# Kernel tuning notes

Hardware: AMD Instinct MI355X
Metric: run time of the kernel (lower is better)

## Reference

```python
import jax, jax.numpy as jnp
import numpy as np

EPS = 1e-7
BLOCK = 64  # block_size from init_kwargs


def project(x):
    norm = jnp.clip(jnp.linalg.norm(x, axis=-1, keepdims=True), EPS)
    return jnp.where(norm >= 1.0, x / norm * (1.0 - EPS), x)


def mobius_add(x, y, c):
    x2 = jnp.sum(x * x, -1, keepdims=True)
    y2 = jnp.sum(y * y, -1, keepdims=True)
    xy = jnp.sum(x * y, -1, keepdims=True)
    num = (1 + 2 * c * xy + c * y2) * x + (1 - c * x2) * y
    den = 1 + 2 * c * xy + c * c * x2 * y2
    return project(num / jnp.clip(den, EPS))


def logmap0(y, c):
    sqrt_c = jnp.clip(jnp.sqrt(c), EPS)
    yn = jnp.linalg.norm(y, axis=-1, keepdims=True)
    mag = jnp.arctanh(jnp.minimum(yn, 1.0 - EPS)) / sqrt_c
    return jnp.where(yn < EPS, jnp.zeros_like(y), mag * (y / jnp.clip(yn, EPS)))


def expmap0(v, c):
    sqrt_c = jnp.clip(jnp.sqrt(c), EPS)
    vn = jnp.linalg.norm(v, axis=-1, keepdims=True)
    mag = jnp.tanh(sqrt_c * jnp.clip(vn, EPS)) / sqrt_c
    return project(jnp.where(vn < EPS, jnp.zeros_like(v), mag * (v / jnp.clip(vn, EPS))))


def pdist(x, y, c):
    # x: [B,H,S,1,D], y: [B,H,1,S,D], c: [1,H,1,1,1] -> [B,H,S,S]
    sqrt_c = jnp.clip(jnp.sqrt(c), EPS)
    add_norm = jnp.linalg.norm(mobius_add(-x, y, c), axis=-1)
    sc = jnp.squeeze(sqrt_c, -1)
    arg = jnp.minimum(sc * add_norm, 1.0 - EPS)
    return 2.0 * jnp.arctanh(arg) / sc


def layernorm(x, scale, bias, eps=1e-6):
    mu = jnp.mean(x, -1, keepdims=True)
    var = jnp.mean(jnp.square(x - mu), -1, keepdims=True)
    return (x - mu) * jax.lax.rsqrt(var + eps) * scale + bias


def precompute_freqs_cis(dim, end, theta=10000.0):
    f = 1.0 / theta ** (jnp.arange(0, dim, 2, dtype=jnp.float32) / dim)
    return jnp.exp(1j * jnp.outer(jnp.arange(end), f))


def rope(x, fc):
    # split-half rotary, as in WubuBlock.apply_rotary_emb
    xr, xi = jnp.split(x, 2, -1)
    xc = jax.lax.complex(xr, xi) * fc.reshape(1, 1, fc.shape[0], fc.shape[1])
    return jnp.concatenate([xc.real, xc.imag], -1)


def setup_inputs() -> dict:
    key = jax.random.key(0)
    ks = jax.random.split(key, 8)
    B, N, D, H = 1, 1024, 512, 8
    w = lambda k, shape, s=0.02: jax.random.normal(k, shape, jnp.float32) * s
    return {
        'x': w(ks[0], (B, N, D), 0.02),  # points well inside the Poincare ball
        'c_global': jax.random.uniform(ks[1], (B, 1), jnp.float32, 0.5, 1.5),
        'W_qkv': w(ks[2], (D, 3 * D)), 'b_qkv': jnp.zeros((3 * D,), jnp.float32),
        'W_out': w(ks[3], (D, D)), 'b_out': jnp.zeros((D,), jnp.float32),
        'ln1_scale': jnp.ones((D,), jnp.float32), 'ln1_bias': jnp.zeros((D,), jnp.float32),
        'ln2_scale': jnp.ones((D,), jnp.float32), 'ln2_bias': jnp.zeros((D,), jnp.float32),
        'W_ff1': w(ks[4], (D, 4 * D)), 'b_ff1': jnp.zeros((4 * D,), jnp.float32),
        'W_ff2': w(ks[5], (4 * D, D)), 'b_ff2': jnp.zeros((D,), jnp.float32),
        'c_per_head_logits': jnp.zeros((H,), jnp.float32),
        'geo_scale': jnp.ones((1, H, 1, 1), jnp.float32),
        'start_pos': 0,
    }


def reference(x, c_global, W_qkv, b_qkv, W_out, b_out, ln1_scale, ln1_bias,
              ln2_scale, ln2_bias, W_ff1, b_ff1, W_ff2, b_ff2,
              c_per_head_logits, geo_scale, start_pos):
    B, N, D = x.shape
    H = c_per_head_logits.shape[0]
    hd = D // H
    S = BLOCK
    nb = N // S
    Be = B * nb
    xb = x.reshape(Be, S, D)
    c_b = jnp.repeat(c_global, nb, axis=0).reshape(Be, 1, 1)

    # tangent-space layernorm (norm1) then logmap to tangent for QKV proj
    xn = expmap0(layernorm(logmap0(xb, c_b), ln1_scale, ln1_bias), c_b)
    xt = logmap0(xn, c_b)
    qkv = (xt @ W_qkv + b_qkv).reshape(Be, S, 3, H, hd).transpose(2, 0, 3, 1, 4)
    q, k, v = qkv[0], qkv[1], qkv[2]  # [Be,H,S,hd]

    fc = precompute_freqs_cis(hd, S)
    q = rope(q, fc)
    k = rope(k, fc)

    c_h = jax.nn.softplus(c_per_head_logits).reshape(1, H, 1, 1)
    qh = expmap0(q, c_h)
    kh = expmap0(k, c_h)

    # full pairwise hyperbolic distance: [Be,H,S,S]
    d = pdist(qh[:, :, :, None, :], kh[:, :, None, :, :], c_h[:, :, None, :, :])
    attn = jax.nn.softmax(-geo_scale * d, axis=-1)
    ao = jnp.einsum('bhqk,bhkd->bhqd', attn, v)
    ao = ao.transpose(0, 2, 1, 3).reshape(Be, S, D)

    ah = expmap0(ao @ W_out + b_out, c_b)
    xa = mobius_add(xb, ah, c_b)  # hyperbolic residual

    # hyperbolic FFN with tangent-space norm (norm2)
    xn2 = expmap0(layernorm(logmap0(xa, c_b), ln2_scale, ln2_bias), c_b)
    t = logmap0(xn2, c_b)
    fh = expmap0(jax.nn.gelu(t @ W_ff1 + b_ff1) @ W_ff2 + b_ff2, c_b)
    out = mobius_add(xa, fh, c_b)
    return out.reshape(B, N, D)
```

## Files before the change

kernel.cpp:

```cpp
#include <hip/hip_runtime.h>
#include <math.h>

#define DEV __device__ __forceinline__
typedef _Float16 h16;
typedef __attribute__((ext_vector_type(8))) _Float16 h8v;
typedef __attribute__((ext_vector_type(4))) _Float16 h4v;
typedef __attribute__((ext_vector_type(4))) float f4v;

constexpr int NTOK = 1024;
constexpr int D    = 512;
constexpr int H    = 8;
constexpr int NB   = 16;
constexpr double EPSd = 1e-7;

DEV double wave_sum(double v) {
#pragma unroll
  for (int m = 32; m; m >>= 1) v += __shfl_xor(v, m, 64);
  return v;
}

DEV void tcast64(const float* __restrict__ src, h16* __restrict__ dst,
                 int K, int N, int n0, int k0, float* tls ) {
  const int tx = threadIdx.x & 15, ty = threadIdx.x >> 4;
#pragma unroll
  for (int it = 0; it < 4; ++it) {
    const int k = ty + it * 16;
    float4 v = *(const float4*)(src + (size_t)(k0 + k) * N + n0 + tx * 4);
    *(float4*)(tls + k * 68 + tx * 4) = v;
  }
  __syncthreads();
#pragma unroll
  for (int it = 0; it < 4; ++it) {
    const int n = ty + it * 16;
    const int kc = tx * 4;
    h4v o;
#pragma unroll
    for (int j = 0; j < 4; ++j) o[j] = (h16)tls[(kc + j) * 68 + n];
    *(h4v*)(dst + (size_t)(n0 + n) * K + k0 + kc) = o;
  }
}

__global__ void k_prep(const float* __restrict__ Wqkv, const float* __restrict__ Wout,
                       const float* __restrict__ Wff1, const float* __restrict__ Wff2,
                       const float* __restrict__ x, const float* __restrict__ cg,
                       const float* __restrict__ s1, const float* __restrict__ b1,
                       h16* __restrict__ qT, h16* __restrict__ oT,
                       h16* __restrict__ f1T, h16* __restrict__ f2T,
                       h16* __restrict__ xt) {
  __shared__ __align__(16) float tls[64 * 68];
  const int bid = blockIdx.x;
  if (bid < 768) {
    const float* src; h16* dst; int K, N, bx, by, l;
    if (bid < 192)      { l = bid;       src = Wqkv; dst = qT;  K = 512;  N = 1536; bx = l % 24; by = l / 24; }
    else if (bid < 256) { l = bid - 192; src = Wout; dst = oT;  K = 512;  N = 512;  bx = l % 8;  by = l / 8;  }
    else if (bid < 512) { l = bid - 256; src = Wff1; dst = f1T; K = 512;  N = 2048; bx = l % 32; by = l / 32; }
    else                { l = bid - 512; src = Wff2; dst = f2T; K = 2048; N = 512;  bx = l % 8;  by = l / 8;  }
    tcast64(src, dst, K, N, bx * 64, by * 64, tls);
    return;
  }
  const int wid = threadIdx.x >> 6, lane = threadIdx.x & 63;
  const int tok = (bid - 768) * 4 + wid;
  const float4* xr = (const float4*)(x + (size_t)tok * D);
  float4 xv0 = xr[lane], xv1 = xr[lane + 64];
  double sv = 0.0, svv = 0.0;
  {
    const float e[8] = {xv0.x, xv0.y, xv0.z, xv0.w, xv1.x, xv1.y, xv1.z, xv1.w};
#pragma unroll
    for (int j = 0; j < 8; ++j) { double d = e[j]; sv += d; svv += d * d; }
  }
  sv = wave_sum(sv); svv = wave_sum(svv);
  double c = (double)cg[0];
  double sc = sqrt(c); if (sc < EPSd) sc = EPSd;
  double yn = sqrt(svv);
  double arg0 = yn; if (arg0 > 1.0 - EPSd) arg0 = 1.0 - EPSd;
  double f = (yn < EPSd) ? 0.0 : atanh(arg0) / sc / fmax(yn, EPSd);
  double mu = f * sv / D;
  double var = f * f * svv / D - mu * mu;
  double rs = 1.0 / sqrt(var + 1e-6);
  const float4* s1r = (const float4*)s1;
  const float4* b1r = (const float4*)b1;
  float4 sA = s1r[lane], sB = s1r[lane + 64];
  float4 bA = b1r[lane], bB = b1r[lane + 64];
  double w[8]; double sww = 0.0;
  {
    const float e[8]  = {xv0.x, xv0.y, xv0.z, xv0.w, xv1.x, xv1.y, xv1.z, xv1.w};
    const float se[8] = {sA.x, sA.y, sA.z, sA.w, sB.x, sB.y, sB.z, sB.w};
    const float be[8] = {bA.x, bA.y, bA.z, bA.w, bB.x, bB.y, bB.z, bB.w};
#pragma unroll
    for (int j = 0; j < 8; ++j) {
      w[j] = (f * (double)e[j] - mu) * rs * (double)se[j] + (double)be[j];
      sww += w[j] * w[j];
    }
  }
  sww = wave_sum(sww);
  double vn = sqrt(sww);
  double F = 0.0;
  if (vn >= EPSd) {
    double mag_e = tanh(sc * fmax(vn, EPSd)) / sc;
    F = atanh(fmin(mag_e, 1.0 - EPSd)) / (sc * vn);
  }
  h16* dst = xt + (size_t)tok * D;
#pragma unroll
  for (int half = 0; half < 2; ++half) {
    h4v o;
#pragma unroll
    for (int e = 0; e < 4; ++e) o[e] = (h16)(float)(F * w[half * 4 + e]);
    *(h4v*)(dst + 4 * (lane + 64 * half)) = o;
  }
}

DEV void stage_tile(const h16* __restrict__ gbase, int rowstride, h16* lds,
                    int wid, int lane) {
#pragma unroll
  for (int j = 0; j < 2; ++j) {
    const int rbase = wid * 16 + j * 8;
    const int grow = rbase + (lane >> 3);
    const int gch = (lane & 7) ^ (lane >> 3);
    const h16* gp = gbase + (size_t)grow * rowstride + gch * 8;
    __builtin_amdgcn_global_load_lds(
        (const __attribute__((address_space(1))) void*)gp,
        (__attribute__((address_space(3))) void*)(lds + rbase * 64), 16, 0, 0);
  }
}
DEV h8v read_frag(const h16* lds, int row, int c) {
  const int p = c ^ (row & 7);
  return *(const h8v*)(lds + row * 64 + p * 8);
}

template <int GELU, int OHALF, int SPLITK>
__global__ __launch_bounds__(256) void k_mm(
    const h16* __restrict__ A, const h16* __restrict__ B,
    const float* __restrict__ bias, float* __restrict__ Cf, h16* __restrict__ Ch,
    int M, int N, int K) {
  __shared__ __align__(16) h16 As[3][64 * 64];
  __shared__ __align__(16) h16 Bs[3][64 * 64];
  const int tid = threadIdx.x;
  const int lane = tid & 63, wid = tid >> 6;
  const int wr = (wid >> 1) * 32, wc = (wid & 1) * 32;
  const int lr = lane & 15, lg = lane >> 4;
  const size_t r0 = (size_t)blockIdx.y * 64, c0 = (size_t)blockIdx.x * 64;
  const int kz = SPLITK ? blockIdx.z : 0;
  const int Keff = SPLITK ? (K >> 1) : K;
  const f4v z = {0.f, 0.f, 0.f, 0.f};
  f4v acc[2][2]; acc[0][0] = z; acc[0][1] = z; acc[1][0] = z; acc[1][1] = z;
  const h16* Abase = A + r0 * K + (size_t)kz * Keff;
  const h16* Bbase = B + c0 * K + (size_t)kz * Keff;
  const int NT = Keff >> 6;
  stage_tile(Abase, K, As[0], wid, lane);
  stage_tile(Bbase, K, Bs[0], wid, lane);
  stage_tile(Abase + 64, K, As[1], wid, lane);
  stage_tile(Bbase + 64, K, Bs[1], wid, lane);
  int cur = 0;
  for (int t = 0; t < NT; ++t) {
    const int pre = (cur == 2) ? 0 : cur + 1;
    const int pre2 = (pre == 2) ? 0 : pre + 1;
    if (t + 2 < NT) {
      stage_tile(Abase + (t + 2) * 64, K, As[pre2], wid, lane);
      stage_tile(Bbase + (t + 2) * 64, K, Bs[pre2], wid, lane);
    }
    const int rem = NT - 1 - t;
    if (rem >= 2)      asm volatile("s_waitcnt vmcnt(8)" ::: "memory");
    else if (rem == 1) asm volatile("s_waitcnt vmcnt(4)" ::: "memory");
    else               asm volatile("s_waitcnt vmcnt(0)" ::: "memory");
    asm volatile("s_barrier" ::: "memory");
    const h16* Ac = As[cur];
    const h16* Bc = Bs[cur];
#pragma unroll
    for (int ks = 0; ks < 2; ++ks) {
      const int c = ks * 4 + lg;
      h8v a0 = read_frag(Ac, wr + lr, c);
      h8v a1 = read_frag(Ac, wr + 16 + lr, c);
      h8v b0 = read_frag(Bc, wc + lr, c);
      h8v b1 = read_frag(Bc, wc + 16 + lr, c);
      acc[0][0] = __builtin_amdgcn_mfma_f32_16x16x32_f16(a0, b0, acc[0][0], 0, 0, 0);
      acc[0][1] = __builtin_amdgcn_mfma_f32_16x16x32_f16(a0, b1, acc[0][1], 0, 0, 0);
      acc[1][0] = __builtin_amdgcn_mfma_f32_16x16x32_f16(a1, b0, acc[1][0], 0, 0, 0);
      acc[1][1] = __builtin_amdgcn_mfma_f32_16x16x32_f16(a1, b1, acc[1][1], 0, 0, 0);
    }
    asm volatile("s_barrier" ::: "memory");
    cur = pre;
  }
  float* Cfo = Cf + (size_t)kz * M * N;
#pragma unroll
  for (int m = 0; m < 2; ++m)
#pragma unroll
    for (int n = 0; n < 2; ++n) {
      const size_t row = r0 + wr + m * 16 + lg * 4;
      const size_t col = c0 + wc + n * 16 + lr;
      const float bv = (SPLITK && kz) ? 0.f : bias[col];
#pragma unroll
      for (int e = 0; e < 4; ++e) {
        float v = acc[m][n][e] + bv;
        if (GELU) {
          float x3 = v * v * v;
          v = 0.5f * v * (1.0f + tanhf(0.7978845608028654f * (v + 0.044715f * x3)));
        }
        if (OHALF) Ch[(row + e) * N + col] = (h16)v;
        else       Cfo[(row + e) * N + col] = v;
      }
    }
}

__global__ __launch_bounds__(256) void k_attn(
    const h16* __restrict__ qkv, const float* __restrict__ chl,
    const float* __restrict__ geo, h16* __restrict__ ao) {
  __shared__ __align__(16) float Qs[32][68];
  __shared__ __align__(16) float Kt[64][68];
  __shared__ __align__(16) float Vs[64][68];
  __shared__ float q2raw[32], k2raw[64];
  __shared__ float q2s[32], k2s[64], fqv[32], fkv[64];
  const int bid = blockIdx.x;
  const int be = bid >> 4, h = (bid >> 1) & 7, q0 = (bid & 1) * 32;
  const int tid = threadIdx.x;
  const double chd = log1p(exp((double)chl[h]));
  const float ch = (float)chd;
  float sc = (float)sqrt(chd); if (sc < 1e-7f) sc = 1e-7f;
  {
    const int s = tid >> 2, jc = (tid & 3) * 8;
    const h16* base = qkv + (size_t)(be * 64 + s) * 1536 + h * 64;
    h8v klo = *(const h8v*)(base + 512 + jc);
    h8v khi = *(const h8v*)(base + 512 + jc + 32);
    h8v vlo = *(const h8v*)(base + 1024 + jc);
    h8v vhi = *(const h8v*)(base + 1024 + jc + 32);
    float racc = 0.f;
#pragma unroll
    for (int j = 0; j < 8; ++j) {
      float ka = (float)klo[j], kb = (float)khi[j];
      racc += ka * ka + kb * kb;
      float fj = expf((float)(jc + j) * -0.2878231366242557f);
      float st, ct; sincosf((float)s * fj, &st, &ct);
      Kt[jc + j][s]      = ka * ct - kb * st;
      Kt[jc + j + 32][s] = ka * st + kb * ct;
    }
    float4 v0, v1;
#pragma unroll
    for (int j = 0; j < 4; ++j) { v0[j] = (float)vlo[j]; v1[j] = (float)vlo[j + 4]; }
    *(float4*)&Vs[s][jc] = v0; *(float4*)&Vs[s][jc + 4] = v1;
#pragma unroll
    for (int j = 0; j < 4; ++j) { v0[j] = (float)vhi[j]; v1[j] = (float)vhi[j + 4]; }
    *(float4*)&Vs[s][jc + 32] = v0; *(float4*)&Vs[s][jc + 36] = v1;
    racc += __shfl_xor(racc, 1, 64);
    racc += __shfl_xor(racc, 2, 64);
    if ((tid & 3) == 0) k2raw[s] = racc;
  }
  if (tid < 128) {
    const int s = tid >> 2, jc = (tid & 3) * 8;
    const h16* base = qkv + (size_t)(be * 64 + q0 + s) * 1536 + h * 64;
    h8v qlo = *(const h8v*)(base + jc);
    h8v qhi = *(const h8v*)(base + jc + 32);
    float racc = 0.f;
    float rl[8], rh[8];
#pragma unroll
    for (int j = 0; j < 8; ++j) {
      float qa = (float)qlo[j], qb = (float)qhi[j];
      racc += qa * qa + qb * qb;
      float fj = expf((float)(jc + j) * -0.2878231366242557f);
      float st, ct; sincosf((float)(q0 + s) * fj, &st, &ct);
      rl[j] = qa * ct - qb * st;
      rh[j] = qa * st + qb * ct;
    }
    *(float4*)&Qs[s][jc]      = {rl[0], rl[1], rl[2], rl[3]};
    *(float4*)&Qs[s][jc + 4]  = {rl[4], rl[5], rl[6], rl[7]};
    *(float4*)&Qs[s][jc + 32] = {rh[0], rh[1], rh[2], rh[3]};
    *(float4*)&Qs[s][jc + 36] = {rh[4], rh[5], rh[6], rh[7]};
    racc += __shfl_xor(racc, 1, 64);
    racc += __shfl_xor(racc, 2, 64);
    if ((tid & 3) == 0) q2raw[s] = racc;
  }
  __syncthreads();
  if (tid < 64) {
    float n = sqrtf(k2raw[tid]);
    float m = tanhf(sc * fmaxf(n, 1e-7f)) / sc;
    float f = (n < 1e-7f) ? 0.f : m / fmaxf(n, 1e-7f);
    if (m >= 1.f) f *= (1.f - 1e-7f) / m;
    float fn = f * n;
    fkv[tid] = f; k2s[tid] = fn * fn;
  } else if (tid < 96) {
    int i = tid - 64;
    float n = sqrtf(q2raw[i]);
    float m = tanhf(sc * fmaxf(n, 1e-7f)) / sc;
    float f = (n < 1e-7f) ? 0.f : m / fmaxf(n, 1e-7f);
    if (m >= 1.f) f *= (1.f - 1e-7f) / m;
    float fn = f * n;
    fqv[i] = f; q2s[i] = fn * fn;
  }
  __syncthreads();
  const int i = tid >> 3, g = tid & 7;
  float gacc[8];
#pragma unroll
  for (int jj = 0; jj < 8; ++jj) gacc[jj] = 0.f;
  for (int d2 = 0; d2 < 64; ++d2) {
    float qv = Qs[i][d2];
    const float4* kp = (const float4*)&Kt[d2][g * 8];
    float4 k0 = kp[0], k1 = kp[1];
    gacc[0] += qv * k0.x; gacc[1] += qv * k0.y; gacc[2] += qv * k0.z; gacc[3] += qv * k0.w;
    gacc[4] += qv * k1.x; gacc[5] += qv * k1.y; gacc[6] += qv * k1.z; gacc[7] += qv * k1.w;
  }
  const float gs = geo[h];
  const float q2 = q2s[i], fqi = fqv[i];
  float lg[8];
  float mx = -1e30f;
#pragma unroll
  for (int jj = 0; jj < 8; ++jj) {
    float gq = fqi * fkv[g * 8 + jj] * gacc[jj];
    float k2 = k2s[g * 8 + jj];
    float A  = 1.f - 2.f * ch * gq + ch * k2;
    float Bv = 1.f - ch * q2;
    float n2 = fmaxf(A * A * q2 - 2.f * A * Bv * gq + Bv * Bv * k2, 0.f);
    float den = fmaxf(1.f - 2.f * ch * gq + ch * ch * q2 * k2, 1e-7f);
    float r = fminf(sqrtf(n2) / den, 1.f - 1e-7f);
    float arg = fminf(sc * r, 1.f - 1e-7f);
    float l = -gs * (2.f * atanhf(arg) / sc);
    lg[jj] = l; mx = fmaxf(mx, l);
  }
  mx = fmaxf(mx, __shfl_xor(mx, 1, 64));
  mx = fmaxf(mx, __shfl_xor(mx, 2, 64));
  mx = fmaxf(mx, __shfl_xor(mx, 4, 64));
  float pv[8]; float sum = 0.f;
#pragma unroll
  for (int jj = 0; jj < 8; ++jj) { pv[jj] = expf(lg[jj] - mx); sum += pv[jj]; }
  sum += __shfl_xor(sum, 1, 64);
  sum += __shfl_xor(sum, 2, 64);
  sum += __shfl_xor(sum, 4, 64);
  float inv = 1.0f / sum;
#pragma unroll
  for (int jj = 0; jj < 8; ++jj) Qs[i][g * 8 + jj] = pv[jj] * inv;
  float oacc[8];
#pragma unroll
  for (int dd = 0; dd < 8; ++dd) oacc[dd] = 0.f;
  for (int jv = 0; jv < 64; ++jv) {
    float p = Qs[i][jv];
    const float4* vp = (const float4*)&Vs[jv][g * 8];
    float4 v0 = vp[0], v1 = vp[1];
    oacc[0] += p * v0.x; oacc[1] += p * v0.y; oacc[2] += p * v0.z; oacc[3] += p * v0.w;
    oacc[4] += p * v1.x; oacc[5] += p * v1.y; oacc[6] += p * v1.z; oacc[7] += p * v1.w;
  }
  h8v ov;
#pragma unroll
  for (int dd = 0; dd < 8; ++dd) ov[dd] = (h16)oacc[dd];
  *(h8v*)(ao + (size_t)(be * 64 + q0 + i) * D + h * 64 + g * 8) = ov;
}

__global__ void k_resid(const float* __restrict__ x, const float* __restrict__ proj,
                        const float* __restrict__ cg, const float* __restrict__ s2,
                        const float* __restrict__ b2, float* __restrict__ xa,
                        h16* __restrict__ t2) {
  const int wid = threadIdx.x >> 6, lane = threadIdx.x & 63;
  const int tok = blockIdx.x * 4 + wid;
  const float4* xr  = (const float4*)(x + (size_t)tok * D);
  const float4* p0r = (const float4*)(proj + (size_t)tok * D);
  const float4* p1r = (const float4*)(proj + (size_t)NTOK * D + (size_t)tok * D);
  float4 xv0 = xr[lane], xv1 = xr[lane + 64];
  float4 pa0 = p0r[lane], pa1 = p0r[lane + 64];
  float4 pb0 = p1r[lane], pb1 = p1r[lane + 64];
  float pe[8], xe[8];
  xe[0]=xv0.x; xe[1]=xv0.y; xe[2]=xv0.z; xe[3]=xv0.w; xe[4]=xv1.x; xe[5]=xv1.y; xe[6]=xv1.z; xe[7]=xv1.w;
  pe[0]=pa0.x+pb0.x; pe[1]=pa0.y+pb0.y; pe[2]=pa0.z+pb0.z; pe[3]=pa0.w+pb0.w;
  pe[4]=pa1.x+pb1.x; pe[5]=pa1.y+pb1.y; pe[6]=pa1.z+pb1.z; pe[7]=pa1.w+pb1.w;
  double sx = 0, sp = 0, xx = 0, pp = 0, xp = 0;
#pragma unroll
  for (int j = 0; j < 8; ++j) {
    double dx = xe[j], dp = pe[j];
    sx += dx; sp += dp; xx += dx * dx; pp += dp * dp; xp += dx * dp;
  }
  sx = wave_sum(sx); sp = wave_sum(sp); xx = wave_sum(xx);
  pp = wave_sum(pp); xp = wave_sum(xp);
  double c = (double)cg[0];
  double sc = sqrt(c); if (sc < EPSd) sc = EPSd;
  double pn = sqrt(pp);
  double me = tanh(sc * fmax(pn, EPSd)) / sc;
  double fs = (pn < EPSd) ? 0.0 : me / fmax(pn, EPSd);
  if (me >= 1.0) fs *= (1.0 - EPSd) / me;
  double y2 = fs * fs * pp, xy = fs * xp;
  double a = 1.0 + 2.0 * c * xy + c * y2;
  double b = 1.0 - c * xx;
  double den = 1.0 + 2.0 * c * xy + c * c * xx * y2;
  if (den < EPSd) den = EPSd;
  double zn = sqrt(fmax(a * a * xx + 2.0 * a * b * xy + b * b * y2, 0.0)) / den;
  double zs = 1.0 / den;
  if (zn >= 1.0) zs *= (1.0 - EPSd) / zn;
  double xan = (zn >= 1.0) ? (1.0 - EPSd) : zn;
  double A0 = zs * a, B0 = zs * b * fs;
  double xav[8];
#pragma unroll
  for (int j = 0; j < 8; ++j) xav[j] = A0 * (double)xe[j] + B0 * (double)pe[j];
  {
    float4 o0 = {(float)xav[0], (float)xav[1], (float)xav[2], (float)xav[3]};
    float4 o1 = {(float)xav[4], (float)xav[5], (float)xav[6], (float)xav[7]};
    float4* xw = (float4*)(xa + (size_t)tok * D);
    xw[lane] = o0; xw[lane + 64] = o1;
  }
  double sxa  = A0 * sx + B0 * sp;
  double sxa2 = A0 * A0 * xx + 2.0 * A0 * B0 * xp + B0 * B0 * pp;
  double fl = 0.0;
  if (xan >= EPSd) fl = atanh(fmin(xan, 1.0 - EPSd)) / (sc * fmax(xan, EPSd));
  double mu = fl * sxa / D;
  double var = fl * fl * sxa2 / D - mu * mu;
  double rs = 1.0 / sqrt(var + 1e-6);
  const float4* s2r = (const float4*)s2;
  const float4* b2r = (const float4*)b2;
  float4 sA = s2r[lane], sB = s2r[lane + 64];
  float4 bA = b2r[lane], bB = b2r[lane + 64];
  const float se[8] = {sA.x, sA.y, sA.z, sA.w, sB.x, sB.y, sB.z, sB.w};
  const float be[8] = {bA.x, bA.y, bA.z, bA.w, bB.x, bB.y, bB.z, bB.w};
  double w[8]; double sww = 0.0;
#pragma unroll
  for (int j = 0; j < 8; ++j) {
    w[j] = (fl * xav[j] - mu) * rs * (double)se[j] + (double)be[j];
    sww += w[j] * w[j];
  }
  sww = wave_sum(sww);
  double vn = sqrt(sww);
  double F = 0.0;
  if (vn >= EPSd) {
    double mag_e = tanh(sc * fmax(vn, EPSd)) / sc;
    F = atanh(fmin(mag_e, 1.0 - EPSd)) / (sc * vn);
  }
  h16* dst = t2 + (size_t)tok * D;
#pragma unroll
  for (int half = 0; half < 2; ++half) {
    h4v o;
#pragma unroll
    for (int e = 0; e < 4; ++e) o[e] = (h16)(float)(F * w[half * 4 + e]);
    *(h4v*)(dst + 4 * (lane + 64 * half)) = o;
  }
}

__global__ void k_final(const float* __restrict__ xa, const float* __restrict__ f2,
                        const float* __restrict__ cg, float* __restrict__ out) {
  const int wid = threadIdx.x >> 6, lane = threadIdx.x & 63;
  const int tok = blockIdx.x * 4 + wid;
  const float4* ar  = (const float4*)(xa + (size_t)tok * D);
  const float4* f0r = (const float4*)(f2 + (size_t)tok * D);
  const float4* f1r = (const float4*)(f2 + (size_t)NTOK * D + (size_t)tok * D);
  float4 xv0 = ar[lane], xv1 = ar[lane + 64];
  float4 pa0 = f0r[lane], pa1 = f0r[lane + 64];
  float4 pb0 = f1r[lane], pb1 = f1r[lane + 64];
  float pe[8], xe[8];
  xe[0]=xv0.x; xe[1]=xv0.y; xe[2]=xv0.z; xe[3]=xv0.w; xe[4]=xv1.x; xe[5]=xv1.y; xe[6]=xv1.z; xe[7]=xv1.w;
  pe[0]=pa0.x+pb0.x; pe[1]=pa0.y+pb0.y; pe[2]=pa0.z+pb0.z; pe[3]=pa0.w+pb0.w;
  pe[4]=pa1.x+pb1.x; pe[5]=pa1.y+pb1.y; pe[6]=pa1.z+pb1.z; pe[7]=pa1.w+pb1.w;
  double xx = 0, pp = 0, xp = 0;
#pragma unroll
  for (int j = 0; j < 8; ++j) {
    double dx = xe[j], dp = pe[j];
    xx += dx * dx; pp += dp * dp; xp += dx * dp;
  }
  xx = wave_sum(xx); pp = wave_sum(pp); xp = wave_sum(xp);
  double c = (double)cg[0];
  double sc = sqrt(c); if (sc < EPSd) sc = EPSd;
  double pn = sqrt(pp);
  double me = tanh(sc * fmax(pn, EPSd)) / sc;
  double fs = (pn < EPSd) ? 0.0 : me / fmax(pn, EPSd);
  if (me >= 1.0) fs *= (1.0 - EPSd) / me;
  double y2 = fs * fs * pp, xy = fs * xp;
  double a = 1.0 + 2.0 * c * xy + c * y2;
  double b = 1.0 - c * xx;
  double den = 1.0 + 2.0 * c * xy + c * c * xx * y2;
  if (den < EPSd) den = EPSd;
  double zn = sqrt(fmax(a * a * xx + 2.0 * a * b * xy + b * b * y2, 0.0)) / den;
  double zs = 1.0 / den;
  if (zn >= 1.0) zs *= (1.0 - EPSd) / zn;
  double A0 = zs * a, B0 = zs * b * fs;
  float4 o0, o1;
  o0.x = (float)(A0 * xe[0] + B0 * pe[0]); o0.y = (float)(A0 * xe[1] + B0 * pe[1]);
  o0.z = (float)(A0 * xe[2] + B0 * pe[2]); o0.w = (float)(A0 * xe[3] + B0 * pe[3]);
  o1.x = (float)(A0 * xe[4] + B0 * pe[4]); o1.y = (float)(A0 * xe[5] + B0 * pe[5]);
  o1.z = (float)(A0 * xe[6] + B0 * pe[6]); o1.w = (float)(A0 * xe[7] + B0 * pe[7]);
  float4* ow = (float4*)(out + (size_t)tok * D);
  ow[lane] = o0; ow[lane + 64] = o1;
}

extern "C" void kernel_launch(void* const* d_in, const int* in_sizes, int n_in,
                              void* d_out, int out_size, void* d_ws, size_t ws_size,
                              hipStream_t stream) {
  (void)in_sizes; (void)n_in; (void)out_size; (void)ws_size;
  const float* x    = (const float*)d_in[0];
  const float* cg   = (const float*)d_in[1];
  const float* Wqkv = (const float*)d_in[2];
  const float* bqkv = (const float*)d_in[3];
  const float* Wout = (const float*)d_in[4];
  const float* bout = (const float*)d_in[5];
  const float* s1   = (const float*)d_in[6];
  const float* b1   = (const float*)d_in[7];
  const float* s2   = (const float*)d_in[8];
  const float* b2   = (const float*)d_in[9];
  const float* Wff1 = (const float*)d_in[10];
  const float* bff1 = (const float*)d_in[11];
  const float* Wff2 = (const float*)d_in[12];
  const float* bff2 = (const float*)d_in[13];
  const float* chl  = (const float*)d_in[14];
  const float* geo  = (const float*)d_in[15];
  float* out = (float*)d_out;

  char* base = (char*)d_ws;
  const size_t MB = 1024 * 1024;
  h16*   WqkvT = (h16*)(base + 0);
  h16*   WoutT = (h16*)(base + (3*MB)/2);
  h16*   Wff1T = (h16*)(base + 2*MB);
  h16*   Wff2T = (h16*)(base + 4*MB);
  h16*   xt    = (h16*)(base + 6*MB);
  h16*   qkv   = (h16*)(base + 7*MB);
  h16*   ao    = (h16*)(base + 10*MB);
  float* proj  = (float*)(base + 11*MB);
  float* xa    = (float*)(base + 7*MB);
  h16*   t2    = (h16*)(base + 6*MB);
  h16*   h1    = (h16*)(base + 11*MB);
  float* f2    = (float*)(base + 0);

  k_prep<<<768 + NTOK / 4, 256, 0, stream>>>(Wqkv, Wout, Wff1, Wff2, x, cg, s1, b1,
                                             WqkvT, WoutT, Wff1T, Wff2T, xt);
  k_mm<0, 1, 0><<<dim3(1536 / 64, NTOK / 64), 256, 0, stream>>>(
      xt, WqkvT, bqkv, nullptr, qkv, NTOK, 1536, 512);
  k_attn<<<NB * H * 2, 256, 0, stream>>>(qkv, chl, geo, ao);
  k_mm<0, 0, 1><<<dim3(512 / 64, NTOK / 64, 2), 256, 0, stream>>>(
      ao, WoutT, bout, proj, nullptr, NTOK, 512, 512);
  k_resid<<<NTOK / 4, 256, 0, stream>>>(x, proj, cg, s2, b2, xa, t2);
  k_mm<1, 1, 0><<<dim3(2048 / 64, NTOK / 64), 256, 0, stream>>>(
      t2, Wff1T, bff1, nullptr, h1, NTOK, 2048, 512);
  k_mm<0, 0, 1><<<dim3(512 / 64, NTOK / 64, 2), 256, 0, stream>>>(
      h1, Wff2T, bff2, f2, nullptr, NTOK, 512, 2048);
  k_final<<<NTOK / 4, 256, 0, stream>>>(xa, f2, cg, out);
}
```

Baseline: 71.06 us.

## Move non-QKV weight transpose-casts into the attention kernel's spare blocks

The transpose-and-cast to fp16 of Wout, Wff1 and Wff2 moves out of the prep kernel and into extra blocks launched alongside the attention kernel, which has only 256 blocks and leaves the GPU underfilled. This shortens the critical-path prep kernel and overlaps weight conversion with attention work, reusing the attention shared buffer as scratch. The GEMM kernel also now loads bias values before the main loop instead of in the epilogue, with a full vmcnt wait that may stall the start slightly.

```diff
diff --git a/kernel.cpp b/kernel.cpp
--- a/kernel.cpp
+++ b/kernel.cpp
@@ -40,26 +40,18 @@
   }
 }
 
-__global__ void k_prep(const float* __restrict__ Wqkv, const float* __restrict__ Wout,
-                       const float* __restrict__ Wff1, const float* __restrict__ Wff2,
+__global__ void k_prep(const float* __restrict__ Wqkv,
                        const float* __restrict__ x, const float* __restrict__ cg,
                        const float* __restrict__ s1, const float* __restrict__ b1,
-                       h16* __restrict__ qT, h16* __restrict__ oT,
-                       h16* __restrict__ f1T, h16* __restrict__ f2T,
-                       h16* __restrict__ xt) {
+                       h16* __restrict__ qT, h16* __restrict__ xt) {
   __shared__ __align__(16) float tls[64 * 68];
   const int bid = blockIdx.x;
-  if (bid < 768) {
-    const float* src; h16* dst; int K, N, bx, by, l;
-    if (bid < 192)      { l = bid;       src = Wqkv; dst = qT;  K = 512;  N = 1536; bx = l % 24; by = l / 24; }
-    else if (bid < 256) { l = bid - 192; src = Wout; dst = oT;  K = 512;  N = 512;  bx = l % 8;  by = l / 8;  }
-    else if (bid < 512) { l = bid - 256; src = Wff1; dst = f1T; K = 512;  N = 2048; bx = l % 32; by = l / 32; }
-    else                { l = bid - 512; src = Wff2; dst = f2T; K = 2048; N = 512;  bx = l % 8;  by = l / 8;  }
-    tcast64(src, dst, K, N, bx * 64, by * 64, tls);
+  if (bid < 192) {
+    tcast64(Wqkv, qT, 512, 1536, (bid % 24) * 64, (bid / 24) * 64, tls);
     return;
   }
   const int wid = threadIdx.x >> 6, lane = threadIdx.x & 63;
-  const int tok = (bid - 768) * 4 + wid;
+  const int tok = (bid - 192) * 4 + wid;
   const float4* xr = (const float4*)(x + (size_t)tok * D);
   float4 xv0 = xr[lane], xv1 = xr[lane + 64];
   double sv = 0.0, svv = 0.0;
@@ -146,6 +138,12 @@
   const h16* Abase = A + r0 * K + (size_t)kz * Keff;
   const h16* Bbase = B + c0 * K + (size_t)kz * Keff;
   const int NT = Keff >> 6;
+  const size_t col0 = c0 + wc + lr;
+  float bv0 = bias[col0];
+  float bv1 = bias[col0 + 16];
+  asm volatile("" :: "v"(bv0), "v"(bv1));
+  asm volatile("s_waitcnt vmcnt(0)" ::: "memory");
+  if (SPLITK && kz) { bv0 = 0.f; bv1 = 0.f; }
   stage_tile(Abase, K, As[0], wid, lane);
   stage_tile(Bbase, K, Bs[0], wid, lane);
   stage_tile(Abase + 64, K, As[1], wid, lane);
@@ -186,8 +184,8 @@
 #pragma unroll
     for (int n = 0; n < 2; ++n) {
       const size_t row = r0 + wr + m * 16 + lg * 4;
-      const size_t col = c0 + wc + n * 16 + lr;
-      const float bv = (SPLITK && kz) ? 0.f : bias[col];
+      const size_t col = col0 + n * 16;
+      const float bv = n ? bv1 : bv0;
 #pragma unroll
       for (int e = 0; e < 4; ++e) {
         float v = acc[m][n][e] + bv;
@@ -203,13 +201,24 @@
 
 __global__ __launch_bounds__(256) void k_attn(
     const h16* __restrict__ qkv, const float* __restrict__ chl,
-    const float* __restrict__ geo, h16* __restrict__ ao) {
+    const float* __restrict__ geo, h16* __restrict__ ao,
+    const float* __restrict__ Wo, const float* __restrict__ Wf1,
+    const float* __restrict__ Wf2,
+    h16* __restrict__ oT, h16* __restrict__ f1T, h16* __restrict__ f2T) {
   __shared__ __align__(16) float Qs[32][68];
   __shared__ __align__(16) float Kt[64][68];
   __shared__ __align__(16) float Vs[64][68];
   __shared__ float q2raw[32], k2raw[64];
   __shared__ float q2s[32], k2s[64], fqv[32], fkv[64];
   const int bid = blockIdx.x;
+  if (bid >= 256) {
+    const float* src; h16* dst; int K, N, bx, by, l;
+    if (bid < 320)      { l = bid - 256; src = Wo;  dst = oT;  K = 512;  N = 512;  bx = l % 8;  by = l / 8;  }
+    else if (bid < 576) { l = bid - 320; src = Wf1; dst = f1T; K = 512;  N = 2048; bx = l % 32; by = l / 32; }
+    else                { l = bid - 576; src = Wf2; dst = f2T; K = 2048; N = 512;  bx = l % 8;  by = l / 8;  }
+    tcast64(src, dst, K, N, bx * 64, by * 64, &Kt[0][0]);
+    return;
+  }
   const int be = bid >> 4, h = (bid >> 1) & 7, q0 = (bid & 1) * 32;
   const int tid = threadIdx.x;
   const double chd = log1p(exp((double)chl[h]));
@@ -508,11 +517,11 @@
   h16*   h1    = (h16*)(base + 11*MB);
   float* f2    = (float*)(base + 0);
 
-  k_prep<<<768 + NTOK / 4, 256, 0, stream>>>(Wqkv, Wout, Wff1, Wff2, x, cg, s1, b1,
-                                             WqkvT, WoutT, Wff1T, Wff2T, xt);
+  k_prep<<<192 + NTOK / 4, 256, 0, stream>>>(Wqkv, x, cg, s1, b1, WqkvT, xt);
   k_mm<0, 1, 0><<<dim3(1536 / 64, NTOK / 64), 256, 0, stream>>>(
       xt, WqkvT, bqkv, nullptr, qkv, NTOK, 1536, 512);
-  k_attn<<<NB * H * 2, 256, 0, stream>>>(qkv, chl, geo, ao);
+  k_attn<<<NB * H * 2 + 576, 256, 0, stream>>>(qkv, chl, geo, ao,
+                                               Wout, Wff1, Wff2, WoutT, Wff1T, Wff2T);
   k_mm<0, 0, 1><<<dim3(512 / 64, NTOK / 64, 2), 256, 0, stream>>>(
       ao, WoutT, bout, proj, nullptr, NTOK, 512, 512);
   k_resid<<<NTOK / 4, 256, 0, stream>>>(x, proj, cg, s2, b2, xa, t2);
```

New measurement: 68.38 us (median of 2 runs). -3.8%, faster.
